# Performance work log

Hardware: AMD Instinct MI355X
Metric: run time of the kernel (lower is better)

## Reference

```python
import jax, jax.numpy as jnp
import numpy as np

B, L, H, E, K, P, V = 32, 64, 1024, 8, 2, 8, 12000
OUT = 2 * P  # moe_gauss out_features
COEF = 0.1   # moe_loss_coef


def setup_inputs() -> dict:
    key = jax.random.key(0)
    ks = jax.random.split(key, 6)
    s = 0.02
    return {
        "query_repr": jax.random.normal(ks[0], (B, H), jnp.float32),
        "h": jax.random.normal(ks[1], (B, L, H), jnp.float32),
        "gate_w1": jax.random.normal(ks[2], (H, H // 2), jnp.float32) * s,
        "gate_b1": jnp.zeros((H // 2,), jnp.float32),
        "gate_w2": jax.random.normal(ks[3], (H // 2, E), jnp.float32) * s,
        "gate_b2": jnp.zeros((E,), jnp.float32),
        "gauss_w": jax.random.normal(ks[4], (E, OUT, H), jnp.float32) * s,
        "gauss_b": jnp.zeros((E, OUT), jnp.float32),
        "comp_w": jax.random.normal(ks[5], (E, V, H), jnp.float32) * s,
        "comp_b": jnp.zeros((E, V), jnp.float32),
    }


def reference(query_repr, h, gate_w1, gate_b1, gate_w2, gate_b2,
              gauss_w, gauss_b, comp_w, comp_b):
    # --- QueryGuidedGating: MLP -> top-k -> softmax -> scatter ---
    hid = jax.nn.relu(query_repr @ gate_w1 + gate_b1)          # [B, H/2]
    logits = hid @ gate_w2 + gate_b2                            # [B, E]
    top_vals, top_idx = jax.lax.top_k(logits, K)                # [B, K]
    top_gates = jax.nn.softmax(top_vals, axis=-1)               # [B, K]
    rows = jnp.arange(logits.shape[0])[:, None]
    gates = jnp.zeros_like(logits).at[rows, top_idx].set(top_gates)  # [B, E]

    # --- balance_loss: cv = std(importance)/(mean+eps) * coef (torch std is ddof=1) ---
    importance = gates.sum(0)                                   # [E]
    moe_loss = (jnp.std(importance, ddof=1) / (importance.mean() + 1e-10)) * COEF

    # --- QueryGuidedMoELinear: per-sample mixed weight, then bmm ---
    mixed_w = jnp.einsum('be,eoi->boi', gates, gauss_w)         # [B, OUT, H]
    mixed_b = jnp.einsum('be,eo->bo', gates, gauss_b)           # [B, OUT]
    h_last = h[:, -1]                                           # [B, H]
    gauss_param = jax.nn.sigmoid(jnp.einsum('bi,boi->bo', h_last, mixed_w) + mixed_b)

    # --- _moe_comp_forward: gated accumulation over experts (avoids [B,E,L,V]) ---
    comp = jnp.zeros((h.shape[0], h.shape[1], comp_w.shape[1]), h.dtype)
    for e in range(E):  # fixed small expert count
        expert_out = jnp.einsum('blh,vh->blv', h, comp_w[e]) + comp_b[e]
        comp = comp + gates[:, e, None, None] * expert_out

    return gauss_param, comp, moe_loss
```

## Files before the change

kernel.cpp:

```cpp
#include <hip/hip_runtime.h>
#include <hip/hip_bf16.h>
#include <cmath>

#define B_   32
#define L_   64
#define H_   1024
#define E_   8
#define V_   12000
#define OUT_ 16
#define HID_ 512

#define BN  96
#define BK  64
#define LDK 72

#define COMP_OFF 512
#define LOSS_OFF (512 + B_ * L_ * V_)

using f32x4  = __attribute__((ext_vector_type(4))) float;
using bf16x8 = __attribute__((ext_vector_type(8))) short;
using s16x4  = __attribute__((ext_vector_type(4))) short;

__device__ __forceinline__ short f2bf(float f) {
  unsigned u = __builtin_bit_cast(unsigned, f);
  u = (u + 0x7FFFu + ((u >> 16) & 1u)) >> 16;
  return (short)u;
}

typedef __attribute__((address_space(1))) void gvoid_t;
typedef __attribute__((address_space(3))) void lvoid_t;
#define GLOAD16(g, l) __builtin_amdgcn_global_load_lds((gvoid_t*)(g), (lvoid_t*)(l), 16, 0, 0)

__global__ __launch_bounds__(256) void k_conv(const float* __restrict__ src,
                                              short* __restrict__ dst, int n8) {
  size_t i = (size_t)blockIdx.x * 256 + threadIdx.x;
  const size_t stride = (size_t)gridDim.x * 256;
  for (; i < (size_t)n8; i += stride) {
    const f32x4 a = ((const f32x4*)src)[2 * i];
    const f32x4 b = ((const f32x4*)src)[2 * i + 1];
    bf16x8 o;
    o[0] = f2bf(a[0]); o[1] = f2bf(a[1]); o[2] = f2bf(a[2]); o[3] = f2bf(a[3]);
    o[4] = f2bf(b[0]); o[5] = f2bf(b[1]); o[6] = f2bf(b[2]); o[7] = f2bf(b[3]);
    ((bf16x8*)dst)[i] = o;
  }
}

__global__ __launch_bounds__(256) void k_gate(
    const float* __restrict__ q,  const float* __restrict__ w1,
    const float* __restrict__ b1, const float* __restrict__ w2,
    const float* __restrict__ b2, const float* __restrict__ h,
    const float* __restrict__ gw, const float* __restrict__ gb,
    float* __restrict__ gates,    float* __restrict__ egate,
    int* __restrict__ eidx,       float* __restrict__ out) {
  __shared__ __align__(16) float qs[H_];
  __shared__ __align__(16) float hid[HID_];
  __shared__ __align__(16) float red[256][8];
  __shared__ float sg[2];
  __shared__ int   se[2];
  const int t = threadIdx.x;
  const int b = blockIdx.x;

  ((f32x4*)qs)[t] = ((const f32x4*)(q + (size_t)b * H_))[t];
  __syncthreads();

  {
    const int jq = t & 127, ih = t >> 7;
    f32x4 acc = {0.f, 0.f, 0.f, 0.f};
    const float* wp = w1 + (size_t)(ih * 512) * HID_ + 4 * jq;
    for (int i = 0; i < 512; ++i) {
      acc += qs[ih * 512 + i] * *(const f32x4*)(wp + (size_t)i * HID_);
    }
    *(f32x4*)&red[t][0] = acc;
  }
  __syncthreads();
  if (t < 128) {
    f32x4 a = *(f32x4*)&red[t][0];
    a += *(f32x4*)&red[t + 128][0];
    a += *(const f32x4*)(b1 + 4 * t);
    f32x4 r;
    #pragma unroll
    for (int c = 0; c < 4; ++c) r[c] = fmaxf(a[c], 0.f);
    *(f32x4*)&hid[4 * t] = r;
  }
  __syncthreads();

  {
    const float h0 = hid[t], h1 = hid[t + 256];
    const float* w2a = w2 + (size_t)t * E_;
    const float* w2b = w2 + (size_t)(t + 256) * E_;
    #pragma unroll
    for (int e = 0; e < 8; ++e) red[t][e] = h0 * w2a[e] + h1 * w2b[e];
  }
  __syncthreads();
  for (int s = 128; s > 0; s >>= 1) {
    if (t < s) {
      #pragma unroll
      for (int e = 0; e < 8; ++e) red[t][e] += red[t + s][e];
    }
    __syncthreads();
  }

  if (t == 0) {
    float lg[8];
    #pragma unroll
    for (int e = 0; e < 8; ++e) lg[e] = red[0][e] + b2[e];
    int e1 = 0;
    #pragma unroll
    for (int e = 1; e < 8; ++e) if (lg[e] > lg[e1]) e1 = e;
    int e2 = (e1 == 0) ? 1 : 0;
    #pragma unroll
    for (int e = 0; e < 8; ++e) if (e != e1 && lg[e] > lg[e2]) e2 = e;
    const float x2 = expf(lg[e2] - lg[e1]);
    const float g1 = 1.f / (1.f + x2);
    const float g2 = x2 / (1.f + x2);
    #pragma unroll
    for (int e = 0; e < 8; ++e)
      gates[b * E_ + e] = (e == e1) ? g1 : (e == e2) ? g2 : 0.f;
    egate[2 * b] = g1; egate[2 * b + 1] = g2;
    eidx[2 * b]  = e1; eidx[2 * b + 1]  = e2;
    sg[0] = g1; sg[1] = g2; se[0] = e1; se[1] = e2;
  }
  __syncthreads();

  {
    const float gg1 = sg[0], gg2 = sg[1];
    const int ee1 = se[0], ee2 = se[1];
    const int o = t >> 4, sub = t & 15;
    const float* hl = h  + ((size_t)(b * L_ + (L_ - 1))) * H_ + sub * 64;
    const float* wa = gw + ((size_t)(ee1 * OUT_ + o)) * H_ + sub * 64;
    const float* wb = gw + ((size_t)(ee2 * OUT_ + o)) * H_ + sub * 64;
    float p = 0.f;
    #pragma unroll 4
    for (int i = 0; i < 64; i += 4) {
      const f32x4 hv = *(const f32x4*)(hl + i);
      const f32x4 va = *(const f32x4*)(wa + i);
      const f32x4 vb = *(const f32x4*)(wb + i);
      const f32x4 w  = gg1 * va + gg2 * vb;
      p += hv[0] * w[0] + hv[1] * w[1] + hv[2] * w[2] + hv[3] * w[3];
    }
    float* red1 = &red[0][0];
    red1[t] = p;
    __syncthreads();
    if (t < 16) {
      float s = gg1 * gb[ee1 * OUT_ + t] + gg2 * gb[ee2 * OUT_ + t];
      #pragma unroll
      for (int k2 = 0; k2 < 16; ++k2) s += red1[t * 16 + k2];
      out[b * OUT_ + t] = 1.f / (1.f + expf(-s));
    }
  }
}

__global__ __launch_bounds__(64) void k_loss(const float* __restrict__ gates,
                                             float* __restrict__ out) {
  __shared__ float imp[8];
  const int t = threadIdx.x;
  if (t < 8) {
    float s = 0.f;
    for (int b = 0; b < B_; ++b) s += gates[b * E_ + t];
    imp[t] = s;
  }
  __syncthreads();
  if (t == 0) {
    float m = 0.f;
    #pragma unroll
    for (int e = 0; e < 8; ++e) m += imp[e];
    m *= 0.125f;
    float var = 0.f;
    #pragma unroll
    for (int e = 0; e < 8; ++e) { const float d = imp[e] - m; var += d * d; }
    var *= (1.f / 7.f);
    out[LOSS_OFF] = sqrtf(var) / (m + 1e-10f) * 0.1f;
  }
}

__global__ __launch_bounds__(256) void k_comp_fast(
    const short* __restrict__ hbf, const short* __restrict__ wbf,
    const float* __restrict__ cb,  const float* __restrict__ egate,
    const int* __restrict__ eidx,  float* __restrict__ out) {
  __shared__ __align__(16) short As [64 * 64];
  __shared__ __align__(16) short Bs1[96 * 64];
  __shared__ __align__(16) short Bs2[96 * 64];
  const int t  = threadIdx.x;
  const int b  = blockIdx.x;
  const int vt = blockIdx.y;
  const int e1 = eidx[2 * b], e2 = eidx[2 * b + 1];
  const float g1 = egate[2 * b], g2 = egate[2 * b + 1];

  const int srow = t >> 3, schunk = t & 7;
  const unsigned sxor = (unsigned)((srow & 7) << 4);
  const unsigned soff = (unsigned)((schunk << 4) ^ sxor);
  const char* sA  = (const char*)hbf + ((size_t)b * 64 + srow) * 2048 + soff;
  const char* sB1 = (const char*)wbf + ((size_t)e1 * V_ + (size_t)vt * 96 + srow) * 2048 + soff;
  const char* sB2 = (const char*)wbf + ((size_t)e2 * V_ + (size_t)vt * 96 + srow) * 2048 + soff;
  char* dA  = (char*)As  + t * 16;
  char* dB1 = (char*)Bs1 + t * 16;
  char* dB2 = (char*)Bs2 + t * 16;

  const int lane = t & 63, wv = t >> 6;
  const int lr = lane & 15, quad = lane >> 4;
  const int mh = wv & 1, ng = wv >> 1;
  int offA[2][2], offB[3][2];
  #pragma unroll
  for (int mf = 0; mf < 2; ++mf) {
    const int ra = mh * 32 + mf * 16 + lr;
    offA[mf][0] = ra * 64 + (((quad    ) ^ (ra & 7)) << 3);
    offA[mf][1] = ra * 64 + (((quad ^ 4) ^ (ra & 7)) << 3);
  }
  #pragma unroll
  for (int nn = 0; nn < 3; ++nn) {
    const int rb = (ng * 3 + nn) * 16 + lr;
    offB[nn][0] = rb * 64 + (((quad    ) ^ (rb & 7)) << 3);
    offB[nn][1] = rb * 64 + (((quad ^ 4) ^ (rb & 7)) << 3);
  }

  f32x4 acc1[2][3], acc2[2][3];
  #pragma unroll
  for (int i = 0; i < 2; ++i)
    #pragma unroll
    for (int j = 0; j < 3; ++j) {
      acc1[i][j] = (f32x4){0.f, 0.f, 0.f, 0.f};
      acc2[i][j] = (f32x4){0.f, 0.f, 0.f, 0.f};
    }

  for (int k0 = 0; k0 < H_; k0 += 64) {
    GLOAD16(sA,           dA);
    GLOAD16(sA + 65536,   dA + 4096);
    GLOAD16(sB1,          dB1);
    GLOAD16(sB1 + 65536,  dB1 + 4096);
    GLOAD16(sB1 + 131072, dB1 + 8192);
    GLOAD16(sB2,          dB2);
    GLOAD16(sB2 + 65536,  dB2 + 4096);
    GLOAD16(sB2 + 131072, dB2 + 8192);
    sA += 128; sB1 += 128; sB2 += 128;
    __syncthreads();

    #pragma unroll
    for (int ks = 0; ks < 2; ++ks) {
      const bf16x8 a0 = *(const bf16x8*)(As + offA[0][ks]);
      const bf16x8 a1 = *(const bf16x8*)(As + offA[1][ks]);
      #pragma unroll
      for (int nn = 0; nn < 3; ++nn) {
        const bf16x8 wb1 = *(const bf16x8*)(Bs1 + offB[nn][ks]);
        acc1[0][nn] = __builtin_amdgcn_mfma_f32_16x16x32_bf16(a0, wb1, acc1[0][nn], 0, 0, 0);
        acc1[1][nn] = __builtin_amdgcn_mfma_f32_16x16x32_bf16(a1, wb1, acc1[1][nn], 0, 0, 0);
        const bf16x8 wb2 = *(const bf16x8*)(Bs2 + offB[nn][ks]);
        acc2[0][nn] = __builtin_amdgcn_mfma_f32_16x16x32_bf16(a0, wb2, acc2[0][nn], 0, 0, 0);
        acc2[1][nn] = __builtin_amdgcn_mfma_f32_16x16x32_bf16(a1, wb2, acc2[1][nn], 0, 0, 0);
      }
    }
    __syncthreads();
  }

  #pragma unroll
  for (int nn = 0; nn < 3; ++nn) {
    const int v = vt * 96 + (ng * 3 + nn) * 16 + lr;
    const float bias = g1 * cb[e1 * V_ + v] + g2 * cb[e2 * V_ + v];
    #pragma unroll
    for (int mf = 0; mf < 2; ++mf) {
      const int lbase = mh * 32 + mf * 16 + quad * 4;
      float* op = out + COMP_OFF + ((size_t)(b * L_ + lbase)) * V_ + v;
      #pragma unroll
      for (int rr = 0; rr < 4; ++rr)
        op[(size_t)rr * V_] = g1 * acc1[mf][nn][rr] + g2 * acc2[mf][nn][rr] + bias;
    }
  }
}

__global__ __launch_bounds__(256) void k_comp(
    const float* __restrict__ h,     const float* __restrict__ cw,
    const float* __restrict__ cbp,   const float* __restrict__ egate,
    const int* __restrict__ eidx,    float* __restrict__ out) {
  __shared__ __align__(16) short As[L_ * LDK];
  __shared__ __align__(16) short Bs[BN * LDK];
  const int t  = threadIdx.x;
  const int b  = blockIdx.x;
  const int vt = blockIdx.y;
  const int e1 = eidx[2 * b], e2 = eidx[2 * b + 1];
  const float g1 = egate[2 * b], g2 = egate[2 * b + 1];

  const float* hrow = h + ((size_t)b * L_ + (t >> 2)) * H_ + ((t & 3) * 16);
  const float* w1p  = cw + ((size_t)e1 * V_ + (size_t)vt * BN) * H_;
  const float* w2p  = cw + ((size_t)e2 * V_ + (size_t)vt * BN) * H_;

  f32x4 acc[6];
  #pragma unroll
  for (int i = 0; i < 6; ++i) acc[i] = (f32x4){0.f, 0.f, 0.f, 0.f};

  const int wv = t >> 6;
  const int lane = t & 63;
  const int lr = lane & 15, quad = lane >> 4;
  const short* Ap = As + (wv * 16 + lr) * LDK;
  const short* Bp = Bs + lr * LDK;

  const int wr = t >> 3;
  const int wc = (t & 7) * 8;

  for (int k0 = 0; k0 < H_; k0 += BK) {
    {
      const float* src = hrow + k0;
      short* dst = As + (t >> 2) * LDK + (t & 3) * 16;
      #pragma unroll
      for (int c = 0; c < 16; c += 4) {
        const f32x4 v = *(const f32x4*)(src + c);
        s16x4 sv;
        sv[0] = f2bf(v[0]); sv[1] = f2bf(v[1]);
        sv[2] = f2bf(v[2]); sv[3] = f2bf(v[3]);
        *(s16x4*)(dst + c) = sv;
      }
    }
    #pragma unroll
    for (int p = 0; p < 3; ++p) {
      const int r = p * 32 + wr;
      const float* s1 = w1p + (size_t)r * H_ + k0 + wc;
      const float* s2 = w2p + (size_t)r * H_ + k0 + wc;
      short* dst = Bs + r * LDK + wc;
      #pragma unroll
      for (int c = 0; c < 8; c += 4) {
        const f32x4 a  = *(const f32x4*)(s1 + c);
        const f32x4 bb = *(const f32x4*)(s2 + c);
        const f32x4 m  = g1 * a + g2 * bb;
        s16x4 sv;
        sv[0] = f2bf(m[0]); sv[1] = f2bf(m[1]);
        sv[2] = f2bf(m[2]); sv[3] = f2bf(m[3]);
        *(s16x4*)(dst + c) = sv;
      }
    }
    __syncthreads();

    #pragma unroll
    for (int ks = 0; ks < BK; ks += 32) {
      const bf16x8 af = *(const bf16x8*)(Ap + ks + quad * 8);
      #pragma unroll
      for (int n = 0; n < 6; ++n) {
        const bf16x8 bf = *(const bf16x8*)(Bp + n * 16 * LDK + ks + quad * 8);
        acc[n] = __builtin_amdgcn_mfma_f32_16x16x32_bf16(af, bf, acc[n], 0, 0, 0);
      }
    }
    __syncthreads();
  }

  #pragma unroll
  for (int n = 0; n < 6; ++n) {
    const int v = vt * BN + n * 16 + lr;
    const float bias = g1 * cbp[e1 * V_ + v] + g2 * cbp[e2 * V_ + v];
    #pragma unroll
    for (int r = 0; r < 4; ++r) {
      const int l = wv * 16 + quad * 4 + r;
      out[COMP_OFF + ((size_t)(b * L_ + l)) * V_ + v] = acc[n][r] + bias;
    }
  }
}

extern "C" void kernel_launch(void* const* d_in, const int* in_sizes, int n_in,
                              void* d_out, int out_size, void* d_ws, size_t ws_size,
                              hipStream_t stream) {
  const float* q   = (const float*)d_in[0];
  const float* h   = (const float*)d_in[1];
  const float* w1  = (const float*)d_in[2];
  const float* b1  = (const float*)d_in[3];
  const float* w2  = (const float*)d_in[4];
  const float* b2  = (const float*)d_in[5];
  const float* gw  = (const float*)d_in[6];
  const float* gb  = (const float*)d_in[7];
  const float* cw  = (const float*)d_in[8];
  const float* cbp = (const float*)d_in[9];
  float* out = (float*)d_out;

  float* F     = (float*)d_ws;
  float* gates = F;
  float* egate = F + 256;
  int*   eidx  = (int*)(F + 320);

  const size_t HBF_OFF = 4096;
  const size_t HBF_BYTES = (size_t)B_ * L_ * H_ * 2;
  const size_t WBF_OFF = HBF_OFF + HBF_BYTES;
  const size_t WBF_BYTES = (size_t)E_ * V_ * H_ * 2;
  const size_t WS_NEED = WBF_OFF + WBF_BYTES;

  k_gate<<<B_, 256, 0, stream>>>(q, w1, b1, w2, b2, h, gw, gb, gates, egate, eidx, out);
  k_loss<<<1, 64, 0, stream>>>(gates, out);

  if (ws_size >= WS_NEED) {
    short* hbf = (short*)((char*)d_ws + HBF_OFF);
    short* wbf = (short*)((char*)d_ws + WBF_OFF);
    k_conv<<<2048, 256, 0, stream>>>(cw, wbf, (int)((size_t)E_ * V_ * H_ / 8));
    k_conv<<<256, 256, 0, stream>>>(h, hbf, (int)((size_t)B_ * L_ * H_ / 8));
    k_comp_fast<<<dim3(B_, V_ / BN), 256, 0, stream>>>(hbf, wbf, cbp, egate, eidx, out);
  } else {
    k_comp<<<dim3(B_, V_ / BN), 256, 0, stream>>>(h, cw, cbp, egate, eidx, out);
  }
}
```

Baseline: 821.3 us.

## Fuse expert weight mixing and bf16 conversion into the comp GEMM

The separate full-weight fp32-to-bf16 conversion pass is removed. Each block now loads the fp32 rows of its two selected experts, blends them with the gate values (g1*W1+g2*W2), converts to bf16 and stores a single B tile in shared memory. This halves the MFMA count and drops the large conversion read and write, at the cost of reading fp32 weights inside the GEMM, which leans on L2/MALL reuse across batches. The A tile is now double buffered and the B global loads are prefetched into registers to overlap memory with compute.

```diff
diff --git a/kernel.cpp b/kernel.cpp
--- a/kernel.cpp
+++ b/kernel.cpp
@@ -174,12 +174,11 @@
 }
 
 __global__ __launch_bounds__(256) void k_comp_fast(
-    const short* __restrict__ hbf, const short* __restrict__ wbf,
+    const short* __restrict__ hbf, const float* __restrict__ cw,
     const float* __restrict__ cb,  const float* __restrict__ egate,
     const int* __restrict__ eidx,  float* __restrict__ out) {
-  __shared__ __align__(16) short As [64 * 64];
-  __shared__ __align__(16) short Bs1[96 * 64];
-  __shared__ __align__(16) short Bs2[96 * 64];
+  __shared__ __align__(16) short As[2][64 * 64];
+  __shared__ __align__(16) short Bs[96 * 64];
   const int t  = threadIdx.x;
   const int b  = blockIdx.x;
   const int vt = blockIdx.y;
@@ -187,14 +186,42 @@
   const float g1 = egate[2 * b], g2 = egate[2 * b + 1];
 
   const int srow = t >> 3, schunk = t & 7;
-  const unsigned sxor = (unsigned)((srow & 7) << 4);
-  const unsigned soff = (unsigned)((schunk << 4) ^ sxor);
-  const char* sA  = (const char*)hbf + ((size_t)b * 64 + srow) * 2048 + soff;
-  const char* sB1 = (const char*)wbf + ((size_t)e1 * V_ + (size_t)vt * 96 + srow) * 2048 + soff;
-  const char* sB2 = (const char*)wbf + ((size_t)e2 * V_ + (size_t)vt * 96 + srow) * 2048 + soff;
-  char* dA  = (char*)As  + t * 16;
-  char* dB1 = (char*)Bs1 + t * 16;
-  char* dB2 = (char*)Bs2 + t * 16;
+  const unsigned soff = (unsigned)((schunk << 4) ^ ((srow & 7) << 4));
+  const char* sAk = (const char*)hbf + ((size_t)b * 64 + srow) * 2048 + soff;
+  char* dA0 = (char*)&As[0][0] + t * 16;
+  char* dA1 = (char*)&As[1][0] + t * 16;
+
+  const float* wB1 = cw + ((size_t)e1 * V_ + (size_t)vt * BN + srow) * H_ + schunk * 8;
+  const float* wB2 = cw + ((size_t)e2 * V_ + (size_t)vt * BN + srow) * H_ + schunk * 8;
+  short* dBp = Bs + srow * 64 + ((schunk ^ (srow & 7)) << 3);
+
+  f32x4 r1[3][2], r2[3][2];
+
+#define LOADB(koff)                                                          \
+  do {                                                                       \
+    _Pragma("unroll")                                                        \
+    for (int p = 0; p < 3; ++p) {                                            \
+      r1[p][0] = *(const f32x4*)(wB1 + (size_t)p * 32 * H_ + (koff));        \
+      r1[p][1] = *(const f32x4*)(wB1 + (size_t)p * 32 * H_ + (koff) + 4);    \
+      r2[p][0] = *(const f32x4*)(wB2 + (size_t)p * 32 * H_ + (koff));        \
+      r2[p][1] = *(const f32x4*)(wB2 + (size_t)p * 32 * H_ + (koff) + 4);    \
+    }                                                                        \
+  } while (0)
+
+#define WRITEB()                                                             \
+  do {                                                                       \
+    _Pragma("unroll")                                                        \
+    for (int p = 0; p < 3; ++p) {                                            \
+      const f32x4 m0 = g1 * r1[p][0] + g2 * r2[p][0];                        \
+      const f32x4 m1 = g1 * r1[p][1] + g2 * r2[p][1];                        \
+      bf16x8 o;                                                              \
+      o[0] = f2bf(m0[0]); o[1] = f2bf(m0[1]);                                \
+      o[2] = f2bf(m0[2]); o[3] = f2bf(m0[3]);                                \
+      o[4] = f2bf(m1[0]); o[5] = f2bf(m1[1]);                                \
+      o[6] = f2bf(m1[2]); o[7] = f2bf(m1[3]);                                \
+      *(bf16x8*)(dBp + p * 32 * 64) = o;                                     \
+    }                                                                        \
+  } while (0)
 
   const int lane = t & 63, wv = t >> 6;
   const int lr = lane & 15, quad = lane >> 4;
@@ -213,39 +240,40 @@
     offB[nn][1] = rb * 64 + (((quad ^ 4) ^ (rb & 7)) << 3);
   }
 
-  f32x4 acc1[2][3], acc2[2][3];
+  f32x4 acc[2][3];
   #pragma unroll
   for (int i = 0; i < 2; ++i)
     #pragma unroll
-    for (int j = 0; j < 3; ++j) {
-      acc1[i][j] = (f32x4){0.f, 0.f, 0.f, 0.f};
-      acc2[i][j] = (f32x4){0.f, 0.f, 0.f, 0.f};
-    }
-
-  for (int k0 = 0; k0 < H_; k0 += 64) {
-    GLOAD16(sA,           dA);
-    GLOAD16(sA + 65536,   dA + 4096);
-    GLOAD16(sB1,          dB1);
-    GLOAD16(sB1 + 65536,  dB1 + 4096);
-    GLOAD16(sB1 + 131072, dB1 + 8192);
-    GLOAD16(sB2,          dB2);
-    GLOAD16(sB2 + 65536,  dB2 + 4096);
-    GLOAD16(sB2 + 131072, dB2 + 8192);
-    sA += 128; sB1 += 128; sB2 += 128;
-    __syncthreads();
-
+    for (int j = 0; j < 3; ++j) acc[i][j] = (f32x4){0.f, 0.f, 0.f, 0.f};
+
+  GLOAD16(sAk,         dA0);
+  GLOAD16(sAk + 65536, dA0 + 4096);
+  sAk += 128;
+  LOADB(0);
+  int koff = 64;
+
+  for (int t16 = 0; t16 < 16; ++t16) {
+    WRITEB();
+    __syncthreads();
+
+    if (t16 < 15) {
+      char* dAn = (t16 & 1) ? dA0 : dA1;
+      GLOAD16(sAk,         dAn);
+      GLOAD16(sAk + 65536, dAn + 4096);
+      sAk += 128;
+      LOADB(koff);
+      koff += 64;
+    }
+    const short* Asb = &As[t16 & 1][0];
     #pragma unroll
     for (int ks = 0; ks < 2; ++ks) {
-      const bf16x8 a0 = *(const bf16x8*)(As + offA[0][ks]);
-      const bf16x8 a1 = *(const bf16x8*)(As + offA[1][ks]);
+      const bf16x8 a0 = *(const bf16x8*)(Asb + offA[0][ks]);
+      const bf16x8 a1 = *(const bf16x8*)(Asb + offA[1][ks]);
       #pragma unroll
       for (int nn = 0; nn < 3; ++nn) {
-        const bf16x8 wb1 = *(const bf16x8*)(Bs1 + offB[nn][ks]);
-        acc1[0][nn] = __builtin_amdgcn_mfma_f32_16x16x32_bf16(a0, wb1, acc1[0][nn], 0, 0, 0);
-        acc1[1][nn] = __builtin_amdgcn_mfma_f32_16x16x32_bf16(a1, wb1, acc1[1][nn], 0, 0, 0);
-        const bf16x8 wb2 = *(const bf16x8*)(Bs2 + offB[nn][ks]);
-        acc2[0][nn] = __builtin_amdgcn_mfma_f32_16x16x32_bf16(a0, wb2, acc2[0][nn], 0, 0, 0);
-        acc2[1][nn] = __builtin_amdgcn_mfma_f32_16x16x32_bf16(a1, wb2, acc2[1][nn], 0, 0, 0);
+        const bf16x8 wbm = *(const bf16x8*)(Bs + offB[nn][ks]);
+        acc[0][nn] = __builtin_amdgcn_mfma_f32_16x16x32_bf16(a0, wbm, acc[0][nn], 0, 0, 0);
+        acc[1][nn] = __builtin_amdgcn_mfma_f32_16x16x32_bf16(a1, wbm, acc[1][nn], 0, 0, 0);
       }
     }
     __syncthreads();
@@ -253,7 +281,7 @@
 
   #pragma unroll
   for (int nn = 0; nn < 3; ++nn) {
-    const int v = vt * 96 + (ng * 3 + nn) * 16 + lr;
+    const int v = vt * BN + (ng * 3 + nn) * 16 + lr;
     const float bias = g1 * cb[e1 * V_ + v] + g2 * cb[e2 * V_ + v];
     #pragma unroll
     for (int mf = 0; mf < 2; ++mf) {
@@ -261,9 +289,11 @@
       float* op = out + COMP_OFF + ((size_t)(b * L_ + lbase)) * V_ + v;
       #pragma unroll
       for (int rr = 0; rr < 4; ++rr)
-        op[(size_t)rr * V_] = g1 * acc1[mf][nn][rr] + g2 * acc2[mf][nn][rr] + bias;
-    }
-  }
+        op[(size_t)rr * V_] = acc[mf][nn][rr] + bias;
+    }
+  }
+#undef LOADB
+#undef WRITEB
 }
 
 __global__ __launch_bounds__(256) void k_comp(
@@ -373,19 +403,15 @@
 
   const size_t HBF_OFF = 4096;
   const size_t HBF_BYTES = (size_t)B_ * L_ * H_ * 2;
-  const size_t WBF_OFF = HBF_OFF + HBF_BYTES;
-  const size_t WBF_BYTES = (size_t)E_ * V_ * H_ * 2;
-  const size_t WS_NEED = WBF_OFF + WBF_BYTES;
+  const size_t WS_NEED = HBF_OFF + HBF_BYTES;
 
   k_gate<<<B_, 256, 0, stream>>>(q, w1, b1, w2, b2, h, gw, gb, gates, egate, eidx, out);
   k_loss<<<1, 64, 0, stream>>>(gates, out);
 
   if (ws_size >= WS_NEED) {
     short* hbf = (short*)((char*)d_ws + HBF_OFF);
-    short* wbf = (short*)((char*)d_ws + WBF_OFF);
-    k_conv<<<2048, 256, 0, stream>>>(cw, wbf, (int)((size_t)E_ * V_ * H_ / 8));
     k_conv<<<256, 256, 0, stream>>>(h, hbf, (int)((size_t)B_ * L_ * H_ / 8));
-    k_comp_fast<<<dim3(B_, V_ / BN), 256, 0, stream>>>(hbf, wbf, cbp, egate, eidx, out);
+    k_comp_fast<<<dim3(B_, V_ / BN), 256, 0, stream>>>(hbf, cw, cbp, egate, eidx, out);
   } else {
     k_comp<<<dim3(B_, V_ / BN), 256, 0, stream>>>(h, cw, cbp, egate, eidx, out);
   }
```

Result: slower. 862.4 us (+5.0%).
